# Performance work log

Measured on AMD Instinct MI355X. Metric: run time of the kernel, lower is better.

## Reference

```python
import jax, jax.numpy as jnp
import numpy as np

L = 26   # num_labels
D = 128  # input_dim


def setup_inputs() -> dict:
    key = jax.random.key(0)
    k1, k2, k3 = jax.random.split(key, 3)
    feat_x = jax.random.normal(k1, (8192, 64, 128), dtype=jnp.float32)
    input_y = jax.random.randint(k2, (8192, 64), 0, L, dtype=jnp.int32)
    # flat params: [L*D emission weights | L*L transition weights]
    params = jax.random.normal(k3, (L * D + L * L,), dtype=jnp.float32) * 0.1
    return {"feat_x": feat_x, "input_y": input_y, "params": params}


def reference(feat_x, input_y, params):
    # Linear-chain CRF negative average log-likelihood:
    #   loss = -mean_b [ score(y_b, x_b) - logZ(x_b) ]
    W = params[: L * D].reshape(L, D)      # emission weights
    Tr = params[L * D :].reshape(L, L)     # transition scores Tr[y_t, y_{t+1}]

    em = jnp.einsum("btd,ld->btl", feat_x, W)  # [B, T, L] emission scores

    # gold path score
    em_score = jnp.take_along_axis(em, input_y[..., None], axis=2)[..., 0].sum(axis=1)  # [B]
    tr_score = Tr[input_y[:, :-1], input_y[:, 1:]].sum(axis=1)                           # [B]

    # partition function via forward algorithm (log-sum-exp DP over time)
    em_t = jnp.swapaxes(em, 0, 1)  # [T, B, L]

    def step(alpha, e_t):
        # alpha: [B, L] log forward messages
        alpha = jax.nn.logsumexp(alpha[:, :, None] + Tr[None, :, :], axis=1) + e_t
        return alpha, None

    alpha_T, _ = jax.lax.scan(step, em_t[0], em_t[1:])
    logZ = jax.nn.logsumexp(alpha_T, axis=1)  # [B]

    return -jnp.mean(em_score + tr_score - logZ)
```

## Files before the change

### kernel.cpp

```cpp
#include <hip/hip_runtime.h>
#include <hip/hip_fp16.h>
#include <hip/hip_bf16.h>

#define NL 26
#define ND 128
#define NT 64
#define NB 8192
#define NIPB 16
#define EMJ 32
#define EMI 16

typedef __attribute__((ext_vector_type(8))) short bf16x8;
typedef __attribute__((ext_vector_type(4))) float f32x4;

__device__ __forceinline__ uint32_t pk_bf16(float lo, float hi) {
    uint32_t r;
    asm("v_cvt_pk_bf16_f32 %0, %1, %2" : "=v"(r) : "v"(lo), "v"(hi));
    return r;
}

__global__ __launch_bounds__(256, 2) void crf_fused(
    const float* __restrict__ X, const int* __restrict__ Y,
    const float* __restrict__ P, float* __restrict__ partials)
{
    __shared__ float TrS[NL * NL];
    __shared__ __half emT[NT][EMJ][EMI];
    __shared__ alignas(16) uint32_t pScr[16][20];
    __shared__ float goldS[NIPB];

    const int tid = threadIdx.x;
    for (int k = tid; k < NL * NL; k += 256) TrS[k] = P[NL * ND + k];
    __syncthreads();

    const int warp = tid >> 6;
    const int lane = tid & 63;
    const int r16  = lane & 15;
    const int kq   = lane >> 4;

    bf16x8 Bf[2][4];
    #pragma unroll
    for (int h = 0; h < 2; ++h) {
        int n = r16 + 16 * h;
        #pragma unroll
        for (int kb = 0; kb < 4; ++kb) {
            float w[8];
            if (n < NL) {
                const float4* wp = reinterpret_cast<const float4*>(P + n * ND + kb * 32 + kq * 8);
                float4 w0 = wp[0], w1 = wp[1];
                w[0]=w0.x; w[1]=w0.y; w[2]=w0.z; w[3]=w0.w;
                w[4]=w1.x; w[5]=w1.y; w[6]=w1.z; w[7]=w1.w;
            } else {
                #pragma unroll
                for (int jj = 0; jj < 8; ++jj) w[jj] = 0.f;
            }
            union { uint32_t u[4]; bf16x8 v; } pk;
            pk.u[0] = pk_bf16(w[0], w[1]); pk.u[1] = pk_bf16(w[2], w[3]);
            pk.u[2] = pk_bf16(w[4], w[5]); pk.u[3] = pk_bf16(w[6], w[7]);
            Bf[h][kb] = pk.v;
        }
    }

    const int item0 = blockIdx.x * NIPB;
    const int tbase = warp * 16;
    const float4* X4 = reinterpret_cast<const float4*>(X);

    auto tile_load = [&](int it, float4 (*xa)[2]) {
        size_t row  = (size_t)(item0 + it) * NT + tbase + r16;
        size_t base = row * 32 + kq * 2;
        #pragma unroll
        for (int kb = 0; kb < 4; ++kb) {
            xa[kb][0] = X4[base + kb * 8];
            xa[kb][1] = X4[base + kb * 8 + 1];
        }
    };
    auto tile_comp = [&](int it, float4 (*xa)[2]) {
        f32x4 acc0 = {0.f,0.f,0.f,0.f}, acc1 = {0.f,0.f,0.f,0.f};
        #pragma unroll
        for (int kb = 0; kb < 4; ++kb) {
            union { uint32_t u[4]; bf16x8 v; } A;
            A.u[0] = pk_bf16(xa[kb][0].x, xa[kb][0].y);
            A.u[1] = pk_bf16(xa[kb][0].z, xa[kb][0].w);
            A.u[2] = pk_bf16(xa[kb][1].x, xa[kb][1].y);
            A.u[3] = pk_bf16(xa[kb][1].z, xa[kb][1].w);
            acc0 = __builtin_amdgcn_mfma_f32_16x16x32_bf16(A.v, Bf[0][kb], acc0, 0, 0, 0);
            acc1 = __builtin_amdgcn_mfma_f32_16x16x32_bf16(A.v, Bf[1][kb], acc1, 0, 0, 0);
        }
        #pragma unroll
        for (int q = 0; q < 4; ++q) {
            int t = tbase + kq * 4 + q;
            emT[t][r16][it]      = __float2half(__expf(acc0[q]) * 0.0625f);
            emT[t][r16 + 16][it] = __float2half(__expf(acc1[q]) * 0.0625f);
        }
    };

    float4 xaA[4][2], xaB[4][2];
    tile_load(0, xaA);
    #pragma unroll 1
    for (int ip = 0; ip < 8; ++ip) {
        int itA = ip * 2, itB = ip * 2 + 1;
        tile_load(itB, xaB);
        tile_comp(itA, xaA);
        if (itB < NIPB - 1) tile_load(itB + 1, xaA);
        tile_comp(itB, xaB);
    }

    __syncthreads();
    if (warp != 0) return;


    {
        const int* yrow = Y + (size_t)(item0 + r16) * NT + kq * 16;
        const int4* y4 = reinterpret_cast<const int4*>(yrow);
        int4 a0 = y4[0], a1 = y4[1], a2 = y4[2], a3 = y4[3];
        int ys[17] = {a0.x,a0.y,a0.z,a0.w, a1.x,a1.y,a1.z,a1.w,
                      a2.x,a2.y,a2.z,a2.w, a3.x,a3.y,a3.z,a3.w, 0};
        if (kq < 3) ys[16] = yrow[16];
        float g = 0.f;
        #pragma unroll
        for (int e = 0; e < 16; ++e) {
            int t = kq * 16 + e;
            g += __logf(__half2float(emT[t][ys[e]][r16]));
            if (t < NT - 1) g += TrS[ys[e] * NL + ys[e + 1]];
        }
        g += __shfl_xor(g, 16);
        g += __shfl_xor(g, 32);
        if (kq == 0) goldS[r16] = g;
    }

    bf16x8 Ef[2];
    #pragma unroll
    for (int h = 0; h < 2; ++h) {
        int n = r16 + 16 * h;
        union { uint32_t u[4]; bf16x8 v; } c;
        #pragma unroll
        for (int w = 0; w < 4; ++w) {
            int s = kq * 4 + w;
            float lo = (n < NL) ? __expf(TrS[s * NL + n]) : 0.f;
            float hi = (n < NL && s + 16 < NL) ? __expf(TrS[(s + 16) * NL + n]) : 0.f;
            c.u[w] = pk_bf16(lo, hi);
        }
        Ef[h] = c.v;
    }

    bf16x8 pfrag;
    {
        union { uint32_t u[4]; bf16x8 v; } c;
        #pragma unroll
        for (int w = 0; w < 4; ++w) {
            int s = kq * 4 + w;
            float lo = __half2float(emT[0][s][r16]);
            float hi = (s + 16 < NL) ? __half2float(emT[0][s + 16][r16]) : 0.f;
            c.u[w] = pk_bf16(lo, hi);
        }
        pfrag = c.v;
    }

    float M[4] = {0.f, 0.f, 0.f, 0.f};
    float pn0[4], pn1[4];
    const f32x4 zacc = {0.f, 0.f, 0.f, 0.f};
    #pragma unroll 1
    for (int t = 1; t < NT; ++t) {
        f32x4 d0 = __builtin_amdgcn_mfma_f32_16x16x32_bf16(pfrag, Ef[0], zacc, 0, 0, 0);
        f32x4 d1 = __builtin_amdgcn_mfma_f32_16x16x32_bf16(pfrag, Ef[1], zacc, 0, 0, 0);
        const __half2* pe0p = reinterpret_cast<const __half2*>(&emT[t][r16][kq * 4]);
        const __half2* pe1p = reinterpret_cast<const __half2*>(&emT[t][r16 + 16][kq * 4]);
        __half2 pe0a = pe0p[0], pe0b = pe0p[1];
        __half2 pe1a = pe1p[0], pe1b = pe1p[1];
        pn0[0] = d0[0] * __low2float(pe0a);  pn0[1] = d0[1] * __high2float(pe0a);
        pn0[2] = d0[2] * __low2float(pe0b);  pn0[3] = d0[3] * __high2float(pe0b);
        pn1[0] = d1[0] * __low2float(pe1a);  pn1[1] = d1[1] * __high2float(pe1a);
        pn1[2] = d1[2] * __low2float(pe1b);  pn1[3] = d1[3] * __high2float(pe1b);

        if ((t & 3) == 0) {
            #pragma unroll
            for (int q = 0; q < 4; ++q) {
                float m = fmaxf(pn0[q], pn1[q]);
                m = fmaxf(m, __shfl_xor(m, 1));
                m = fmaxf(m, __shfl_xor(m, 2));
                m = fmaxf(m, __shfl_xor(m, 4));
                m = fmaxf(m, __shfl_xor(m, 8));
                float r = __builtin_amdgcn_rcpf(m);
                pn0[q] *= r; pn1[q] *= r;
                M[q] += __logf(m);
            }
        }
        #pragma unroll
        for (int q = 0; q < 4; ++q)
            pScr[kq * 4 + q][r16] = pk_bf16(pn0[q], pn1[q]);
        uint4 pw = *reinterpret_cast<const uint4*>(&pScr[r16][kq * 4]);
        union { uint4 u; bf16x8 v; } pc; pc.u = pw;
        pfrag = pc.v;
    }

    float tot = 0.f;
    #pragma unroll
    for (int q = 0; q < 4; ++q) {
        float s = pn0[q] + pn1[q];
        s += __shfl_xor(s, 1);
        s += __shfl_xor(s, 2);
        s += __shfl_xor(s, 4);
        s += __shfl_xor(s, 8);
        float logZ = M[q] + __logf(s);
        tot += goldS[kq * 4 + q] - logZ;
    }
    tot += __shfl_xor(tot, 16);
    tot += __shfl_xor(tot, 32);
    if (lane == 0) partials[blockIdx.x] = tot;
}

__global__ void crf_reduce2(const float* __restrict__ partials,
                            float* __restrict__ out, int n) {
    __shared__ float red[256];
    float s = 0.f;
    for (int i = threadIdx.x; i < n; i += 256) s += partials[i];
    red[threadIdx.x] = s;
    __syncthreads();
    for (int k = 128; k >= 1; k >>= 1) {
        if ((int)threadIdx.x < k) red[threadIdx.x] += red[threadIdx.x + k];
        __syncthreads();
    }
    if (threadIdx.x == 0) out[0] = -red[0] / (float)NB;
}

extern "C" void kernel_launch(void* const* d_in, const int* in_sizes, int n_in,
                              void* d_out, int out_size, void* d_ws, size_t ws_size,
                              hipStream_t stream) {
    const float* X = (const float*)d_in[0];
    const int*   Y = (const int*)d_in[1];
    const float* P = (const float*)d_in[2];
    float* out = (float*)d_out;
    float* partials = (float*)d_ws;

    crf_fused<<<NB / NIPB, 256, 0, stream>>>(X, Y, P, partials);
    crf_reduce2<<<1, 256, 0, stream>>>(partials, out, NB / NIPB);
}
```

Measured before the change: 70.86 us.

## Overlap emission GEMM with forward recursion via warp specialization and shared-memory flags

```diff
diff --git a/kernel.cpp b/kernel.cpp
--- a/kernel.cpp
+++ b/kernel.cpp
@@ -7,8 +7,6 @@
 #define NT 64
 #define NB 8192
 #define NIPB 16
-#define EMJ 32
-#define EMI 16
 
 typedef __attribute__((ext_vector_type(8))) short bf16x8;
 typedef __attribute__((ext_vector_type(4))) float f32x4;
@@ -19,16 +17,17 @@
     return r;
 }
 
-__global__ __launch_bounds__(256, 2) void crf_fused(
+__global__ __launch_bounds__(256) void crf_fused(
     const float* __restrict__ X, const int* __restrict__ Y,
     const float* __restrict__ P, float* __restrict__ partials)
 {
     __shared__ float TrS[NL * NL];
-    __shared__ __half emT[NT][EMJ][EMI];
+    __shared__ __half emT[NT][32][NIPB];
     __shared__ alignas(16) uint32_t pScr[16][20];
-    __shared__ float goldS[NIPB];
+    __shared__ int ready[4];
 
     const int tid = threadIdx.x;
+    if (tid < 4) ready[tid] = 0;
     for (int k = tid; k < NL * NL; k += 256) TrS[k] = P[NL * ND + k];
     __syncthreads();
 
@@ -36,95 +35,83 @@
     const int lane = tid & 63;
     const int r16  = lane & 15;
     const int kq   = lane >> 4;
-
-    bf16x8 Bf[2][4];
-    #pragma unroll
-    for (int h = 0; h < 2; ++h) {
-        int n = r16 + 16 * h;
+    const int item0 = blockIdx.x * NIPB;
+
+    if (warp > 0) {
+        bf16x8 Bf[2][4];
         #pragma unroll
-        for (int kb = 0; kb < 4; ++kb) {
-            float w[8];
-            if (n < NL) {
-                const float4* wp = reinterpret_cast<const float4*>(P + n * ND + kb * 32 + kq * 8);
-                float4 w0 = wp[0], w1 = wp[1];
-                w[0]=w0.x; w[1]=w0.y; w[2]=w0.z; w[3]=w0.w;
-                w[4]=w1.x; w[5]=w1.y; w[6]=w1.z; w[7]=w1.w;
-            } else {
-                #pragma unroll
-                for (int jj = 0; jj < 8; ++jj) w[jj] = 0.f;
-            }
-            union { uint32_t u[4]; bf16x8 v; } pk;
-            pk.u[0] = pk_bf16(w[0], w[1]); pk.u[1] = pk_bf16(w[2], w[3]);
-            pk.u[2] = pk_bf16(w[4], w[5]); pk.u[3] = pk_bf16(w[6], w[7]);
-            Bf[h][kb] = pk.v;
-        }
-    }
-
-    const int item0 = blockIdx.x * NIPB;
-    const int tbase = warp * 16;
-    const float4* X4 = reinterpret_cast<const float4*>(X);
-
-    auto tile_load = [&](int it, float4 (*xa)[2]) {
-        size_t row  = (size_t)(item0 + it) * NT + tbase + r16;
-        size_t base = row * 32 + kq * 2;
-        #pragma unroll
-        for (int kb = 0; kb < 4; ++kb) {
-            xa[kb][0] = X4[base + kb * 8];
-            xa[kb][1] = X4[base + kb * 8 + 1];
-        }
-    };
-    auto tile_comp = [&](int it, float4 (*xa)[2]) {
-        f32x4 acc0 = {0.f,0.f,0.f,0.f}, acc1 = {0.f,0.f,0.f,0.f};
-        #pragma unroll
-        for (int kb = 0; kb < 4; ++kb) {
-            union { uint32_t u[4]; bf16x8 v; } A;
-            A.u[0] = pk_bf16(xa[kb][0].x, xa[kb][0].y);
-            A.u[1] = pk_bf16(xa[kb][0].z, xa[kb][0].w);
-            A.u[2] = pk_bf16(xa[kb][1].x, xa[kb][1].y);
-            A.u[3] = pk_bf16(xa[kb][1].z, xa[kb][1].w);
-            acc0 = __builtin_amdgcn_mfma_f32_16x16x32_bf16(A.v, Bf[0][kb], acc0, 0, 0, 0);
-            acc1 = __builtin_amdgcn_mfma_f32_16x16x32_bf16(A.v, Bf[1][kb], acc1, 0, 0, 0);
-        }
-        #pragma unroll
-        for (int q = 0; q < 4; ++q) {
-            int t = tbase + kq * 4 + q;
-            emT[t][r16][it]      = __float2half(__expf(acc0[q]) * 0.0625f);
-            emT[t][r16 + 16][it] = __float2half(__expf(acc1[q]) * 0.0625f);
-        }
-    };
-
-    float4 xaA[4][2], xaB[4][2];
-    tile_load(0, xaA);
-    #pragma unroll 1
-    for (int ip = 0; ip < 8; ++ip) {
-        int itA = ip * 2, itB = ip * 2 + 1;
-        tile_load(itB, xaB);
-        tile_comp(itA, xaA);
-        if (itB < NIPB - 1) tile_load(itB + 1, xaA);
-        tile_comp(itB, xaB);
-    }
-
-    __syncthreads();
-    if (warp != 0) return;
-
-
-    {
-        const int* yrow = Y + (size_t)(item0 + r16) * NT + kq * 16;
-        const int4* y4 = reinterpret_cast<const int4*>(yrow);
-        int4 a0 = y4[0], a1 = y4[1], a2 = y4[2], a3 = y4[3];
-        int ys[17] = {a0.x,a0.y,a0.z,a0.w, a1.x,a1.y,a1.z,a1.w,
-                      a2.x,a2.y,a2.z,a2.w, a3.x,a3.y,a3.z,a3.w, 0};
-        if (kq < 3) ys[16] = yrow[16];
-        float g = 0.f;
-        #pragma unroll
-        for (int e = 0; e < 16; ++e) {
-            int t = kq * 16 + e;
-            g += __logf(__half2float(emT[t][ys[e]][r16]));
-            if (t < NT - 1) g += TrS[ys[e] * NL + ys[e + 1]];
-        }
-        g += __shfl_xor(g, 16);
-        g += __shfl_xor(g, 32);
-        if (kq == 0) goldS[r16] = g;
+        for (int h = 0; h < 2; ++h) {
+            int n = r16 + 16 * h;
+            #pragma unroll
+            for (int kb = 0; kb < 4; ++kb) {
+                float w[8];
+                if (n < NL) {
+                    const float4* wp = reinterpret_cast<const float4*>(P + n * ND + kb * 32 + kq * 8);
+                    float4 w0 = wp[0], w1 = wp[1];
+                    w[0]=w0.x; w[1]=w0.y; w[2]=w0.z; w[3]=w0.w;
+                    w[4]=w1.x; w[5]=w1.y; w[6]=w1.z; w[7]=w1.w;
+                } else {
+                    #pragma unroll
+                    for (int jj = 0; jj < 8; ++jj) w[jj] = 0.f;
+                }
+                union { uint32_t u[4]; bf16x8 v; } pk;
+                pk.u[0] = pk_bf16(w[0], w[1]); pk.u[1] = pk_bf16(w[2], w[3]);
+                pk.u[2] = pk_bf16(w[4], w[5]); pk.u[3] = pk_bf16(w[6], w[7]);
+                Bf[h][kb] = pk.v;
+            }
+        }
+
+        const float4* X4 = reinterpret_cast<const float4*>(X);
+        const int ibeg = (warp == 1) ? 0 : (warp == 2) ? 6 : 11;
+        const int cnt  = (warp == 1) ? 6 : 5;
+
+        auto tile_load = [&](int it, int s, float4 (*xa)[2]) {
+            size_t row  = (size_t)(item0 + it) * NT + s * 16 + r16;
+            size_t base = row * 32 + kq * 2;
+            #pragma unroll
+            for (int kb = 0; kb < 4; ++kb) {
+                xa[kb][0] = X4[base + kb * 8];
+                xa[kb][1] = X4[base + kb * 8 + 1];
+            }
+        };
+        auto tile_comp = [&](int it, int s, float4 (*xa)[2]) {
+            f32x4 acc0 = {0.f,0.f,0.f,0.f}, acc1 = {0.f,0.f,0.f,0.f};
+            #pragma unroll
+            for (int kb = 0; kb < 4; ++kb) {
+                union { uint32_t u[4]; bf16x8 v; } A;
+                A.u[0] = pk_bf16(xa[kb][0].x, xa[kb][0].y);
+                A.u[1] = pk_bf16(xa[kb][0].z, xa[kb][0].w);
+                A.u[2] = pk_bf16(xa[kb][1].x, xa[kb][1].y);
+                A.u[3] = pk_bf16(xa[kb][1].z, xa[kb][1].w);
+                acc0 = __builtin_amdgcn_mfma_f32_16x16x32_bf16(A.v, Bf[0][kb], acc0, 0, 0, 0);
+                acc1 = __builtin_amdgcn_mfma_f32_16x16x32_bf16(A.v, Bf[1][kb], acc1, 0, 0, 0);
+            }
+            #pragma unroll
+            for (int q = 0; q < 4; ++q) {
+                int t = s * 16 + kq * 4 + q;
+                emT[t][r16][it]      = __float2half(__expf(acc0[q]) * 0.0625f);
+                emT[t][r16 + 16][it] = __float2half(__expf(acc1[q]) * 0.0625f);
+            }
+        };
+
+        float4 xaA[4][2], xaB[4][2];
+        const int ntile = 4 * cnt;
+        tile_load(ibeg, 0, xaA);
+        #pragma unroll 1
+        for (int li = 0; li < ntile; ++li) {
+            int s = li / cnt, k = li - s * cnt;
+            int lj = li + 1;
+            if (lj < ntile) {
+                int s2 = lj / cnt, k2 = lj - s2 * cnt;
+                tile_load(ibeg + k2, s2, (li & 1) ? xaA : xaB);
+            }
+            tile_comp(ibeg + k, s, (li & 1) ? xaB : xaA);
+            if (k == cnt - 1) {
+                __threadfence_block();
+                if (lane == 0) atomicAdd(&ready[s], 1);
+            }
+        }
+        return;
     }
 
     bf16x8 Ef[2];
@@ -142,66 +129,94 @@
         Ef[h] = c.v;
     }
 
-    bf16x8 pfrag;
-    {
-        union { uint32_t u[4]; bf16x8 v; } c;
-        #pragma unroll
-        for (int w = 0; w < 4; ++w) {
-            int s = kq * 4 + w;
-            float lo = __half2float(emT[0][s][r16]);
-            float hi = (s + 16 < NL) ? __half2float(emT[0][s + 16][r16]) : 0.f;
-            c.u[w] = pk_bf16(lo, hi);
-        }
-        pfrag = c.v;
-    }
-
+    const int* yb = Y + (size_t)(item0 + r16) * NT;
+    float gold = 0.f;
     float M[4] = {0.f, 0.f, 0.f, 0.f};
     float pn0[4], pn1[4];
+    bf16x8 pfrag;
     const f32x4 zacc = {0.f, 0.f, 0.f, 0.f};
+
     #pragma unroll 1
-    for (int t = 1; t < NT; ++t) {
-        f32x4 d0 = __builtin_amdgcn_mfma_f32_16x16x32_bf16(pfrag, Ef[0], zacc, 0, 0, 0);
-        f32x4 d1 = __builtin_amdgcn_mfma_f32_16x16x32_bf16(pfrag, Ef[1], zacc, 0, 0, 0);
-        const __half2* pe0p = reinterpret_cast<const __half2*>(&emT[t][r16][kq * 4]);
-        const __half2* pe1p = reinterpret_cast<const __half2*>(&emT[t][r16 + 16][kq * 4]);
-        __half2 pe0a = pe0p[0], pe0b = pe0p[1];
-        __half2 pe1a = pe1p[0], pe1b = pe1p[1];
-        pn0[0] = d0[0] * __low2float(pe0a);  pn0[1] = d0[1] * __high2float(pe0a);
-        pn0[2] = d0[2] * __low2float(pe0b);  pn0[3] = d0[3] * __high2float(pe0b);
-        pn1[0] = d1[0] * __low2float(pe1a);  pn1[1] = d1[1] * __high2float(pe1a);
-        pn1[2] = d1[2] * __low2float(pe1b);  pn1[3] = d1[3] * __high2float(pe1b);
-
-        if ((t & 3) == 0) {
-            #pragma unroll
-            for (int q = 0; q < 4; ++q) {
-                float m = fmaxf(pn0[q], pn1[q]);
-                m = fmaxf(m, __shfl_xor(m, 1));
-                m = fmaxf(m, __shfl_xor(m, 2));
-                m = fmaxf(m, __shfl_xor(m, 4));
-                m = fmaxf(m, __shfl_xor(m, 8));
-                float r = __builtin_amdgcn_rcpf(m);
-                pn0[q] *= r; pn1[q] *= r;
-                M[q] += __logf(m);
-            }
-        }
-        #pragma unroll
-        for (int q = 0; q < 4; ++q)
-            pScr[kq * 4 + q][r16] = pk_bf16(pn0[q], pn1[q]);
-        uint4 pw = *reinterpret_cast<const uint4*>(&pScr[r16][kq * 4]);
-        union { uint4 u; bf16x8 v; } pc; pc.u = pw;
-        pfrag = pc.v;
-    }
+    for (int s = 0; s < 4; ++s) {
+        volatile int* rp = (volatile int*)&ready[s];
+        while (*rp < 3) __builtin_amdgcn_s_sleep(4);
+        __threadfence_block();
+
+        {
+            int tb = s * 16 + kq * 4;
+            int4 a = *reinterpret_cast<const int4*>(yb + tb);
+            int ynext = (tb + 4 < NT) ? yb[tb + 4] : 0;
+            int ys[5] = {a.x, a.y, a.z, a.w, ynext};
+            #pragma unroll
+            for (int e = 0; e < 4; ++e) {
+                int t = tb + e;
+                gold += __logf(__half2float(emT[t][ys[e]][r16]));
+                if (t < NT - 1) gold += TrS[ys[e] * NL + ys[e + 1]];
+            }
+        }
+
+        int t = s * 16;
+        if (s == 0) {
+            union { uint32_t u[4]; bf16x8 v; } c;
+            #pragma unroll
+            for (int w = 0; w < 4; ++w) {
+                int sl = kq * 4 + w;
+                float lo = __half2float(emT[0][sl][r16]);
+                float hi = (sl + 16 < NL) ? __half2float(emT[0][sl + 16][r16]) : 0.f;
+                c.u[w] = pk_bf16(lo, hi);
+            }
+            pfrag = c.v;
+            t = 1;
+        }
+        const int tend = s * 16 + 16;
+        #pragma unroll 1
+        for (; t < tend; ++t) {
+            f32x4 d0 = __builtin_amdgcn_mfma_f32_16x16x32_bf16(pfrag, Ef[0], zacc, 0, 0, 0);
+            f32x4 d1 = __builtin_amdgcn_mfma_f32_16x16x32_bf16(pfrag, Ef[1], zacc, 0, 0, 0);
+            const __half2* pe0p = reinterpret_cast<const __half2*>(&emT[t][r16][kq * 4]);
+            const __half2* pe1p = reinterpret_cast<const __half2*>(&emT[t][r16 + 16][kq * 4]);
+            __half2 pe0a = pe0p[0], pe0b = pe0p[1];
+            __half2 pe1a = pe1p[0], pe1b = pe1p[1];
+            pn0[0] = d0[0] * __low2float(pe0a);  pn0[1] = d0[1] * __high2float(pe0a);
+            pn0[2] = d0[2] * __low2float(pe0b);  pn0[3] = d0[3] * __high2float(pe0b);
+            pn1[0] = d1[0] * __low2float(pe1a);  pn1[1] = d1[1] * __high2float(pe1a);
+            pn1[2] = d1[2] * __low2float(pe1b);  pn1[3] = d1[3] * __high2float(pe1b);
+
+            if ((t & 3) == 0) {
+                #pragma unroll
+                for (int q = 0; q < 4; ++q) {
+                    float m = fmaxf(pn0[q], pn1[q]);
+                    m = fmaxf(m, __shfl_xor(m, 1));
+                    m = fmaxf(m, __shfl_xor(m, 2));
+                    m = fmaxf(m, __shfl_xor(m, 4));
+                    m = fmaxf(m, __shfl_xor(m, 8));
+                    float r = __builtin_amdgcn_rcpf(m);
+                    pn0[q] *= r; pn1[q] *= r;
+                    M[q] += __logf(m);
+                }
+            }
+            #pragma unroll
+            for (int q = 0; q < 4; ++q)
+                pScr[kq * 4 + q][r16] = pk_bf16(pn0[q], pn1[q]);
+            uint4 pw = *reinterpret_cast<const uint4*>(&pScr[r16][kq * 4]);
+            union { uint4 u; bf16x8 v; } pc; pc.u = pw;
+            pfrag = pc.v;
+        }
+    }
+
+    gold += __shfl_xor(gold, 16);
+    gold += __shfl_xor(gold, 32);
 
     float tot = 0.f;
     #pragma unroll
     for (int q = 0; q < 4; ++q) {
-        float s = pn0[q] + pn1[q];
-        s += __shfl_xor(s, 1);
-        s += __shfl_xor(s, 2);
-        s += __shfl_xor(s, 4);
-        s += __shfl_xor(s, 8);
-        float logZ = M[q] + __logf(s);
-        tot += goldS[kq * 4 + q] - logZ;
+        float ssum = pn0[q] + pn1[q];
+        ssum += __shfl_xor(ssum, 1);
+        ssum += __shfl_xor(ssum, 2);
+        ssum += __shfl_xor(ssum, 4);
+        ssum += __shfl_xor(ssum, 8);
+        float logZ = M[q] + __logf(ssum);
+        tot += __shfl(gold, kq * 4 + q) - logZ;
     }
     tot += __shfl_xor(tot, 16);
     tot += __shfl_xor(tot, 32);
```

Measured after the change: 131.9 us. 1.86x slower.
